# Optimization experiments

Measured on AMD Instinct MI355X. Metric: run time of the kernel, lower is better.

Reference implementation:

```python
import jax, jax.numpy as jnp
import numpy as np

B, T, IN, H, OUT = 1024, 512, 19, 128, 7


def setup_inputs() -> dict:
    key = jax.random.key(0)
    ks = jax.random.split(key, 12)
    k = 1.0 / np.sqrt(H)  # torch default init bound for LSTMCell/Linear
    u = lambda kk, shape: jax.random.uniform(kk, shape, jnp.float32, -k, k)
    return {
        "x": jax.random.normal(ks[0], (B, T, IN), jnp.float32),
        "W_ih1": u(ks[1], (4 * H, IN)),
        "W_hh1": u(ks[2], (4 * H, H)),
        "b_ih1": u(ks[3], (4 * H,)),
        "b_hh1": u(ks[4], (4 * H,)),
        "W_ih2": u(ks[5], (4 * H, H)),
        "W_hh2": u(ks[6], (4 * H, H)),
        "b_ih2": u(ks[7], (4 * H,)),
        "b_hh2": u(ks[8], (4 * H,)),
        "W_lin": u(ks[9], (OUT, H)),
        "b_lin": u(ks[10], (OUT,)),
    }


def _lstm_cell(x_t, h, c, W_ih, W_hh, b_ih, b_hh):
    # gates in torch order: i, f, g, o
    gates = x_t @ W_ih.T + b_ih + h @ W_hh.T + b_hh  # [B, 4H]
    i, f, g, o = jnp.split(gates, 4, axis=-1)
    c_new = jax.nn.sigmoid(f) * c + jax.nn.sigmoid(i) * jnp.tanh(g)
    h_new = jax.nn.sigmoid(o) * jnp.tanh(c_new)
    return h_new, c_new


def reference(x, W_ih1, W_hh1, b_ih1, b_hh1, W_ih2, W_hh2, b_ih2, b_hh2, W_lin, b_lin):
    n = x.shape[0]
    z = jnp.zeros((n, H), jnp.float32)

    def step(carry, x_t):
        h1, c1, h2, c2 = carry
        h1, c1 = _lstm_cell(x_t, h1, c1, W_ih1, W_hh1, b_ih1, b_hh1)
        h2, c2 = _lstm_cell(h1, h2, c2, W_ih2, W_hh2, b_ih2, b_hh2)
        y = h2 @ W_lin.T + b_lin  # [B, OUT]
        return (h1, c1, h2, c2), y

    xs = jnp.swapaxes(x, 0, 1)  # [T, B, IN]
    _, ys = jax.lax.scan(step, (z, z, z, z), xs)  # ys: [T, B, OUT]
    # torch.cat(outputs, 1) -> [B, T*OUT]
    return jnp.swapaxes(ys, 0, 1).reshape(n, -1)
```

## Files before the change

### kernel.cpp

```cpp
#include <hip/hip_runtime.h>


typedef _Float16 half8 __attribute__((ext_vector_type(8)));
typedef float f32x4 __attribute__((ext_vector_type(4)));

#define MFMA16(a, b, c) __builtin_amdgcn_mfma_f32_16x16x32_f16((a), (b), (c), 0, 0, 0)
#define BARRIER() asm volatile("s_waitcnt lgkmcnt(0)\ns_barrier" ::: "memory")

__device__ __forceinline__ void pin(half8& v) { asm volatile("" : "+v"(v)); }

__device__ __forceinline__ float sigf(float x) {
  return __builtin_amdgcn_rcpf(1.f + __expf(-x));
}
__device__ __forceinline__ float tanhf_(float x) {
  return 1.f - 2.f * __builtin_amdgcn_rcpf(1.f + __expf(2.f * x));
}
__device__ __forceinline__ float sel4(const f32x4 a, const int lg) {
  const float v01 = (lg & 1) ? a[1] : a[0];
  const float v23 = (lg & 1) ? a[3] : a[2];
  return (lg & 2) ? v23 : v01;
}

__global__ __launch_bounds__(512) void lstm_layer1_kernel(
    const float* __restrict__ x,
    const float* __restrict__ Wih,
    const float* __restrict__ Whh,
    const float* __restrict__ bih, const float* __restrict__ bhh,
    _Float16* __restrict__ h1g)
{
  __shared__ _Float16 xls[512][12][8];
  __shared__ _Float16 hbuf[2][64][8];
  const int tid = threadIdx.x, bid = blockIdx.x;
  const int wv = tid >> 6, lane = tid & 63;
  const int lg = lane >> 4, lc = lane & 15;
  const int col = wv * 16 + lc;
  const int off0 = lg * 32 + (lc & 3) * 8;
  const int woff = ((wv * 2 + (lc >> 3)) * 4 + lg) * 8 + (lc & 7);

  half8 wih_f[4], whh_f[4][4];
  float bias[4];
#pragma unroll
  for (int g = 0; g < 4; ++g) {
    const int n = g * 128 + col;
    bias[g] = bih[n] + bhh[n];
    half8 f;
#pragma unroll
    for (int j = 0; j < 8; ++j) {
      const int k = lg * 8 + j;
      f[j] = (_Float16)((k < 19) ? Wih[n * 19 + k] : 0.f);
    }
    wih_f[g] = f;
#pragma unroll
    for (int kk = 0; kk < 4; ++kk) {
      const float* p = Whh + n * 128 + kk * 32 + lg * 8;
      half8 f2;
#pragma unroll
      for (int j = 0; j < 8; ++j) f2[j] = (_Float16)p[j];
      whh_f[g][kk] = f2;
    }
  }

  for (int i2 = tid; i2 < 512 * 96; i2 += 512) {
    const int t = i2 / 96, r = i2 - t * 96;
    const int cc = r >> 5, rr = (r >> 3) & 3, j = r & 7;
    const int k = cc * 8 + j;
    float v = 0.f;
    if (k < 19) v = x[((size_t)(bid * 4 + rr) * 512 + t) * 19 + k];
    xls[t][cc * 4 + rr][j] = (_Float16)v;
  }
  for (int i = tid; i < 1024; i += 512) ((_Float16*)hbuf)[i] = (_Float16)0.f;
  __syncthreads();

  float c = 0.f;
  _Float16* h1p = h1g + (size_t)(bid * 4 + lg) * 128 + col;
  const _Float16* xb = &xls[0][0][0] + off0;
  _Float16* hb0p = &hbuf[0][0][0];
  const f32x4 fz = {0.f, 0.f, 0.f, 0.f};
  const bool xv = (lg < 3);

#define L1_STEP(T, RD, WR)                                                    \
  {                                                                           \
    const _Float16* rd = (RD) + off0;                                         \
    const half8 hb0 = *(const half8*)(rd);                                    \
    const half8 hb1 = *(const half8*)(rd + 128);                              \
    const half8 hb2 = *(const half8*)(rd + 256);                              \
    const half8 hb3 = *(const half8*)(rd + 384);                              \
    half8 ax = {};                                                            \
    if (xv) ax = *(const half8*)(xb + (T) * 96);                              \
    f32x4 a0 = MFMA16(ax, wih_f[0], fz);                                      \
    f32x4 a1 = MFMA16(ax, wih_f[1], fz);                                      \
    f32x4 a2 = MFMA16(ax, wih_f[2], fz);                                      \
    f32x4 a3 = MFMA16(ax, wih_f[3], fz);                                      \
    a0 = MFMA16(hb0, whh_f[0][0], a0); a1 = MFMA16(hb0, whh_f[1][0], a1);     \
    a2 = MFMA16(hb0, whh_f[2][0], a2); a3 = MFMA16(hb0, whh_f[3][0], a3);     \
    a0 = MFMA16(hb1, whh_f[0][1], a0); a1 = MFMA16(hb1, whh_f[1][1], a1);     \
    a2 = MFMA16(hb1, whh_f[2][1], a2); a3 = MFMA16(hb1, whh_f[3][1], a3);     \
    a0 = MFMA16(hb2, whh_f[0][2], a0); a1 = MFMA16(hb2, whh_f[1][2], a1);     \
    a2 = MFMA16(hb2, whh_f[2][2], a2); a3 = MFMA16(hb2, whh_f[3][2], a3);     \
    a0 = MFMA16(hb3, whh_f[0][3], a0); a1 = MFMA16(hb3, whh_f[1][3], a1);     \
    a2 = MFMA16(hb3, whh_f[2][3], a2); a3 = MFMA16(hb3, whh_f[3][3], a3);     \
    const float gi = sel4(a0, lg) + bias[0];                                  \
    const float gf = sel4(a1, lg) + bias[1];                                  \
    const float gg = sel4(a2, lg) + bias[2];                                  \
    const float go = sel4(a3, lg) + bias[3];                                  \
    const float I = sigf(gi), F = sigf(gf), G = tanhf_(gg), O = sigf(go);     \
    c = F * c + I * G;                                                        \
    const float h = O * tanhf_(c);                                            \
    const _Float16 h16 = (_Float16)h;                                         \
    (WR)[woff] = h16;                                                         \
    h1p[(size_t)(T) * 131072] = h16;                                          \
    BARRIER();                                                                \
  }

#pragma unroll 1
  for (int t = 0; t < 512; t += 2) {
    L1_STEP(t, hb0p + 512, hb0p);
    L1_STEP(t + 1, hb0p, hb0p + 512);
  }
#undef L1_STEP
}

__global__ __attribute__((amdgpu_waves_per_eu(2, 2))) __launch_bounds__(512)
void lstm_layer2_kernel(
    const _Float16* __restrict__ h1g,
    const float* __restrict__ Wih,
    const float* __restrict__ Whh,
    const float* __restrict__ bih, const float* __restrict__ bhh,
    const float* __restrict__ Wlin,
    const float* __restrict__ blin,
    float* __restrict__ out)
{
  __shared__ _Float16 hbuf[2][512];
  __shared__ _Float16 wlls[16][136];
  const int tid = threadIdx.x, bid = blockIdx.x;
  const int wv = tid >> 6, lane = tid & 63;
  const int lg = lane >> 4, lc = lane & 15;
  const int col = wv * 16 + lc;
  const int off0 = lg * 32 + (lc & 3) * 8;
  const int woff = ((col >> 3) * 4 + lg) * 8 + (col & 7);

  half8 wi_f[4][4], wh_f[4][4];
  float bias_s[4];
#pragma unroll
  for (int g = 0; g < 4; ++g) {
    const int n = g * 128 + col;
    bias_s[g] = bih[n] + bhh[n];
#pragma unroll
    for (int kk = 0; kk < 4; ++kk) {
      const float* pi = Wih + n * 128 + kk * 32 + lg * 8;
      const float* ph = Whh + n * 128 + kk * 32 + lg * 8;
      half8 fi, fh;
#pragma unroll
      for (int j = 0; j < 8; ++j) { fi[j] = (_Float16)pi[j]; fh[j] = (_Float16)ph[j]; }
      wi_f[g][kk] = fi;
      wh_f[g][kk] = fh;
    }
    pin(wi_f[g][0]); pin(wi_f[g][1]); pin(wi_f[g][2]); pin(wi_f[g][3]);
    pin(wh_f[g][0]); pin(wh_f[g][1]); pin(wh_f[g][2]); pin(wh_f[g][3]);
  }
  const f32x4 bV0 = {bias_s[0], bias_s[0], bias_s[0], bias_s[0]};
  const f32x4 bV1 = {bias_s[1], bias_s[1], bias_s[1], bias_s[1]};
  const f32x4 bV2 = {bias_s[2], bias_s[2], bias_s[2], bias_s[2]};
  const f32x4 bV3 = {bias_s[3], bias_s[3], bias_s[3], bias_s[3]};
  const bool yv = (lc < 7);
  const float ybias = yv ? blin[lc] : 0.f;
  const f32x4 ybV = {ybias, ybias, ybias, ybias};

  for (int i = tid; i < 16 * 128; i += 512)
    wlls[i >> 7][i & 127] = (_Float16)((i < 7 * 128) ? Wlin[i] : 0.f);
  for (int i = tid; i < 1024; i += 512) ((_Float16*)hbuf)[i] = (_Float16)0.f;
  __syncthreads();

  float c = 0.f;
  const _Float16* h1p = h1g + (size_t)(bid * 4 + (lc & 3)) * 128 + lg * 8;
  const f32x4 fz = {0.f, 0.f, 0.f, 0.f};
  half8 iC0 = *(const half8*)(h1p), iC1 = *(const half8*)(h1p + 32);
  half8 iC2 = *(const half8*)(h1p + 64), iC3 = *(const half8*)(h1p + 96);

#pragma unroll 1
  for (int t = 0; t < 512; ++t) {
    const int pb = t & 1;
    const _Float16* rd = &hbuf[pb ^ 1][0] + off0;
    const half8 hb0 = *(const half8*)(rd);
    const half8 hb1 = *(const half8*)(rd + 128);
    const half8 hb2 = *(const half8*)(rd + 256);
    const half8 hb3 = *(const half8*)(rd + 384);
    const size_t tn = (size_t)((t + 1 < 512) ? t + 1 : t) * 131072;
    const half8 iN0 = *(const half8*)(h1p + tn);
    const half8 iN1 = *(const half8*)(h1p + tn + 32);
    const half8 iN2 = *(const half8*)(h1p + tn + 64);
    const half8 iN3 = *(const half8*)(h1p + tn + 96);
    f32x4 a0 = MFMA16(iC0, wi_f[0][0], bV0);
    f32x4 a1 = MFMA16(iC0, wi_f[1][0], bV1);
    f32x4 a2 = MFMA16(iC0, wi_f[2][0], bV2);
    f32x4 a3 = MFMA16(iC0, wi_f[3][0], bV3);
    f32x4 b0 = MFMA16(hb0, wh_f[0][0], fz);
    f32x4 b1 = MFMA16(hb0, wh_f[1][0], fz);
    f32x4 b2 = MFMA16(hb0, wh_f[2][0], fz);
    f32x4 b3 = MFMA16(hb0, wh_f[3][0], fz);
    a0 = MFMA16(iC1, wi_f[0][1], a0); a1 = MFMA16(iC1, wi_f[1][1], a1);
    a2 = MFMA16(iC1, wi_f[2][1], a2); a3 = MFMA16(iC1, wi_f[3][1], a3);
    b0 = MFMA16(hb1, wh_f[0][1], b0); b1 = MFMA16(hb1, wh_f[1][1], b1);
    b2 = MFMA16(hb1, wh_f[2][1], b2); b3 = MFMA16(hb1, wh_f[3][1], b3);
    a0 = MFMA16(iC2, wi_f[0][2], a0); a1 = MFMA16(iC2, wi_f[1][2], a1);
    a2 = MFMA16(iC2, wi_f[2][2], a2); a3 = MFMA16(iC2, wi_f[3][2], a3);
    b0 = MFMA16(hb2, wh_f[0][2], b0); b1 = MFMA16(hb2, wh_f[1][2], b1);
    b2 = MFMA16(hb2, wh_f[2][2], b2); b3 = MFMA16(hb2, wh_f[3][2], b3);
    a0 = MFMA16(iC3, wi_f[0][3], a0); a1 = MFMA16(iC3, wi_f[1][3], a1);
    a2 = MFMA16(iC3, wi_f[2][3], a2); a3 = MFMA16(iC3, wi_f[3][3], a3);
    b0 = MFMA16(hb3, wh_f[0][3], b0); b1 = MFMA16(hb3, wh_f[1][3], b1);
    b2 = MFMA16(hb3, wh_f[2][3], b2); b3 = MFMA16(hb3, wh_f[3][3], b3);
    if (wv == 0 && t > 0) {
      const _Float16* wlp = &wlls[lc][0] + lg * 8;
      const half8 w0 = *(const half8*)(wlp);
      const half8 w1 = *(const half8*)(wlp + 32);
      const half8 w2 = *(const half8*)(wlp + 64);
      const half8 w3 = *(const half8*)(wlp + 96);
      f32x4 ya = ybV;
      ya = MFMA16(hb0, w0, ya);
      ya = MFMA16(hb1, w1, ya);
      ya = MFMA16(hb2, w2, ya);
      ya = MFMA16(hb3, w3, ya);
      if (lg == 0 && yv) {
#pragma unroll
        for (int j = 0; j < 4; ++j)
          out[(size_t)(bid * 4 + j) * 3584 + (size_t)(t - 1) * 7 + lc] = ya[j];
      }
    }
    const f32x4 s0 = a0 + b0, s1 = a1 + b1, s2 = a2 + b2, s3 = a3 + b3;
    const float gi = sel4(s0, lg), gf = sel4(s1, lg);
    const float gg = sel4(s2, lg), go = sel4(s3, lg);
    const float I = sigf(gi), F = sigf(gf), G = tanhf_(gg), O = sigf(go);
    c = F * c + I * G;
    hbuf[pb][woff] = (_Float16)(O * tanhf_(c));
    iC0 = iN0; iC1 = iN1; iC2 = iN2; iC3 = iN3;
    BARRIER();
  }

  if (wv == 0) {
    const _Float16* rd = &hbuf[1][0] + off0;
    const half8 hb0 = *(const half8*)(rd);
    const half8 hb1 = *(const half8*)(rd + 128);
    const half8 hb2 = *(const half8*)(rd + 256);
    const half8 hb3 = *(const half8*)(rd + 384);
    const _Float16* wlp = &wlls[lc][0] + lg * 8;
    const half8 w0 = *(const half8*)(wlp);
    const half8 w1 = *(const half8*)(wlp + 32);
    const half8 w2 = *(const half8*)(wlp + 64);
    const half8 w3 = *(const half8*)(wlp + 96);
    f32x4 ya = ybV;
    ya = MFMA16(hb0, w0, ya);
    ya = MFMA16(hb1, w1, ya);
    ya = MFMA16(hb2, w2, ya);
    ya = MFMA16(hb3, w3, ya);
    if (lg == 0 && yv) {
#pragma unroll
      for (int j = 0; j < 4; ++j)
        out[(size_t)(bid * 4 + j) * 3584 + (size_t)511 * 7 + lc] = ya[j];
    }
  }
}

extern "C" void kernel_launch(void* const* d_in, const int* in_sizes, int n_in,
                              void* d_out, int out_size, void* d_ws, size_t ws_size,
                              hipStream_t stream) {
  (void)in_sizes; (void)n_in; (void)out_size; (void)ws_size;
  const float* x     = (const float*)d_in[0];
  const float* W_ih1 = (const float*)d_in[1];
  const float* W_hh1 = (const float*)d_in[2];
  const float* b_ih1 = (const float*)d_in[3];
  const float* b_hh1 = (const float*)d_in[4];
  const float* W_ih2 = (const float*)d_in[5];
  const float* W_hh2 = (const float*)d_in[6];
  const float* b_ih2 = (const float*)d_in[7];
  const float* b_hh2 = (const float*)d_in[8];
  const float* W_lin = (const float*)d_in[9];
  const float* b_lin = (const float*)d_in[10];
  float* out = (float*)d_out;
  _Float16* h1g = (_Float16*)d_ws;

  lstm_layer1_kernel<<<256, 512, 0, stream>>>(x, W_ih1, W_hh1, b_ih1, b_hh1, h1g);
  lstm_layer2_kernel<<<256, 512, 0, stream>>>(h1g, W_ih2, W_hh2, b_ih2, b_hh2,
                                              W_lin, b_lin, out);
}
```

Baseline: 815.9 us.

## Split layer-2 LSTM into producer and consumer waves with an LDS ring

Layer 2 now runs 1024 threads per block. Eight producer waves compute the input projection W_ih·h1 a few steps ahead and write it as fp16 into a 5-slot shared-memory ring. Eight consumer waves then do only the recurrent W_hh MFMAs plus the gate math. This takes the input-projection MFMAs and global loads off the serial recurrence path, but it adds a block-wide barrier that spans twice as many waves. Rounding the pre-activations to fp16 also costs some precision.

```diff
diff --git a/kernel.cpp b/kernel.cpp
--- a/kernel.cpp
+++ b/kernel.cpp
@@ -2,10 +2,13 @@
 
 
 typedef _Float16 half8 __attribute__((ext_vector_type(8)));
+typedef _Float16 half4 __attribute__((ext_vector_type(4)));
 typedef float f32x4 __attribute__((ext_vector_type(4)));
 
 #define MFMA16(a, b, c) __builtin_amdgcn_mfma_f32_16x16x32_f16((a), (b), (c), 0, 0, 0)
 #define BARRIER() asm volatile("s_waitcnt lgkmcnt(0)\ns_barrier" ::: "memory")
+#define D_AHEAD 4
+#define NSLOT 5
 
 __device__ __forceinline__ void pin(half8& v) { asm volatile("" : "+v"(v)); }
 
@@ -120,8 +123,7 @@
 #undef L1_STEP
 }
 
-__global__ __attribute__((amdgpu_waves_per_eu(2, 2))) __launch_bounds__(512)
-void lstm_layer2_kernel(
+__global__ __launch_bounds__(1024) void lstm_layer2_pc(
     const _Float16* __restrict__ h1g,
     const float* __restrict__ Wih,
     const float* __restrict__ Whh,
@@ -130,133 +132,170 @@
     const float* __restrict__ blin,
     float* __restrict__ out)
 {
-  __shared__ _Float16 hbuf[2][512];
+  __shared__ _Float16 ring[NSLOT][2048];
+  __shared__ _Float16 h2b[2][512];
   __shared__ _Float16 wlls[16][136];
   const int tid = threadIdx.x, bid = blockIdx.x;
   const int wv = tid >> 6, lane = tid & 63;
   const int lg = lane >> 4, lc = lane & 15;
-  const int col = wv * 16 + lc;
+  const bool isCons = (wv < 8);
+  const int cw = isCons ? wv : (wv - 8);
+  const int col = cw * 16 + lc;
   const int off0 = lg * 32 + (lc & 3) * 8;
   const int woff = ((col >> 3) * 4 + lg) * 8 + (col & 7);
 
-  half8 wi_f[4][4], wh_f[4][4];
-  float bias_s[4];
-#pragma unroll
-  for (int g = 0; g < 4; ++g) {
-    const int n = g * 128 + col;
-    bias_s[g] = bih[n] + bhh[n];
-#pragma unroll
-    for (int kk = 0; kk < 4; ++kk) {
-      const float* pi = Wih + n * 128 + kk * 32 + lg * 8;
-      const float* ph = Whh + n * 128 + kk * 32 + lg * 8;
-      half8 fi, fh;
-#pragma unroll
-      for (int j = 0; j < 8; ++j) { fi[j] = (_Float16)pi[j]; fh[j] = (_Float16)ph[j]; }
-      wi_f[g][kk] = fi;
-      wh_f[g][kk] = fh;
-    }
-    pin(wi_f[g][0]); pin(wi_f[g][1]); pin(wi_f[g][2]); pin(wi_f[g][3]);
-    pin(wh_f[g][0]); pin(wh_f[g][1]); pin(wh_f[g][2]); pin(wh_f[g][3]);
-  }
-  const f32x4 bV0 = {bias_s[0], bias_s[0], bias_s[0], bias_s[0]};
-  const f32x4 bV1 = {bias_s[1], bias_s[1], bias_s[1], bias_s[1]};
-  const f32x4 bV2 = {bias_s[2], bias_s[2], bias_s[2], bias_s[2]};
-  const f32x4 bV3 = {bias_s[3], bias_s[3], bias_s[3], bias_s[3]};
-  const bool yv = (lc < 7);
-  const float ybias = yv ? blin[lc] : 0.f;
-  const f32x4 ybV = {ybias, ybias, ybias, ybias};
-
-  for (int i = tid; i < 16 * 128; i += 512)
+  for (int i = tid; i < 16 * 128; i += 1024)
     wlls[i >> 7][i & 127] = (_Float16)((i < 7 * 128) ? Wlin[i] : 0.f);
-  for (int i = tid; i < 1024; i += 512) ((_Float16*)hbuf)[i] = (_Float16)0.f;
-  __syncthreads();
-
-  float c = 0.f;
-  const _Float16* h1p = h1g + (size_t)(bid * 4 + (lc & 3)) * 128 + lg * 8;
-  const f32x4 fz = {0.f, 0.f, 0.f, 0.f};
-  half8 iC0 = *(const half8*)(h1p), iC1 = *(const half8*)(h1p + 32);
-  half8 iC2 = *(const half8*)(h1p + 64), iC3 = *(const half8*)(h1p + 96);
-
+  for (int i = tid; i < 1024; i += 1024) ((_Float16*)h2b)[i] = (_Float16)0.f;
+
+  if (isCons) {
+    half8 wh_f[4][4];
+#pragma unroll
+    for (int g = 0; g < 4; ++g) {
+      const int n = g * 128 + col;
+#pragma unroll
+      for (int kk = 0; kk < 4; ++kk) {
+        const float* p = Whh + n * 128 + kk * 32 + lg * 8;
+        half8 f;
+#pragma unroll
+        for (int j = 0; j < 8; ++j) f[j] = (_Float16)p[j];
+        wh_f[g][kk] = f;
+      }
+      pin(wh_f[g][0]); pin(wh_f[g][1]); pin(wh_f[g][2]); pin(wh_f[g][3]);
+    }
+    const bool yv = (lc < 7);
+    const float ybias = yv ? blin[lc] : 0.f;
+    __syncthreads();
+
+    float c = 0.f;
+    int slotR = 0;
 #pragma unroll 1
-  for (int t = 0; t < 512; ++t) {
-    const int pb = t & 1;
-    const _Float16* rd = &hbuf[pb ^ 1][0] + off0;
-    const half8 hb0 = *(const half8*)(rd);
-    const half8 hb1 = *(const half8*)(rd + 128);
-    const half8 hb2 = *(const half8*)(rd + 256);
-    const half8 hb3 = *(const half8*)(rd + 384);
-    const size_t tn = (size_t)((t + 1 < 512) ? t + 1 : t) * 131072;
-    const half8 iN0 = *(const half8*)(h1p + tn);
-    const half8 iN1 = *(const half8*)(h1p + tn + 32);
-    const half8 iN2 = *(const half8*)(h1p + tn + 64);
-    const half8 iN3 = *(const half8*)(h1p + tn + 96);
-    f32x4 a0 = MFMA16(iC0, wi_f[0][0], bV0);
-    f32x4 a1 = MFMA16(iC0, wi_f[1][0], bV1);
-    f32x4 a2 = MFMA16(iC0, wi_f[2][0], bV2);
-    f32x4 a3 = MFMA16(iC0, wi_f[3][0], bV3);
-    f32x4 b0 = MFMA16(hb0, wh_f[0][0], fz);
-    f32x4 b1 = MFMA16(hb0, wh_f[1][0], fz);
-    f32x4 b2 = MFMA16(hb0, wh_f[2][0], fz);
-    f32x4 b3 = MFMA16(hb0, wh_f[3][0], fz);
-    a0 = MFMA16(iC1, wi_f[0][1], a0); a1 = MFMA16(iC1, wi_f[1][1], a1);
-    a2 = MFMA16(iC1, wi_f[2][1], a2); a3 = MFMA16(iC1, wi_f[3][1], a3);
-    b0 = MFMA16(hb1, wh_f[0][1], b0); b1 = MFMA16(hb1, wh_f[1][1], b1);
-    b2 = MFMA16(hb1, wh_f[2][1], b2); b3 = MFMA16(hb1, wh_f[3][1], b3);
-    a0 = MFMA16(iC2, wi_f[0][2], a0); a1 = MFMA16(iC2, wi_f[1][2], a1);
-    a2 = MFMA16(iC2, wi_f[2][2], a2); a3 = MFMA16(iC2, wi_f[3][2], a3);
-    b0 = MFMA16(hb2, wh_f[0][2], b0); b1 = MFMA16(hb2, wh_f[1][2], b1);
-    b2 = MFMA16(hb2, wh_f[2][2], b2); b3 = MFMA16(hb2, wh_f[3][2], b3);
-    a0 = MFMA16(iC3, wi_f[0][3], a0); a1 = MFMA16(iC3, wi_f[1][3], a1);
-    a2 = MFMA16(iC3, wi_f[2][3], a2); a3 = MFMA16(iC3, wi_f[3][3], a3);
-    b0 = MFMA16(hb3, wh_f[0][3], b0); b1 = MFMA16(hb3, wh_f[1][3], b1);
-    b2 = MFMA16(hb3, wh_f[2][3], b2); b3 = MFMA16(hb3, wh_f[3][3], b3);
-    if (wv == 0 && t > 0) {
+    for (int it = 0; it < 512 + D_AHEAD; ++it) {
+      if (it >= D_AHEAD) {
+        const int t = it - D_AHEAD;
+        const int pb = t & 1;
+        const _Float16* rd = &h2b[pb ^ 1][0] + off0;
+        const half8 q0 = *(const half8*)(rd);
+        const half8 q1 = *(const half8*)(rd + 128);
+        const half8 q2 = *(const half8*)(rd + 256);
+        const half8 q3 = *(const half8*)(rd + 384);
+        const _Float16* rp = &ring[slotR][0] + (col << 2);
+        const half4 r0 = *(const half4*)(rp);
+        const half4 r1 = *(const half4*)(rp + 512);
+        const half4 r2 = *(const half4*)(rp + 1024);
+        const half4 r3 = *(const half4*)(rp + 1536);
+        f32x4 a0 = {(float)r0[0], (float)r0[1], (float)r0[2], (float)r0[3]};
+        f32x4 a1 = {(float)r1[0], (float)r1[1], (float)r1[2], (float)r1[3]};
+        f32x4 a2 = {(float)r2[0], (float)r2[1], (float)r2[2], (float)r2[3]};
+        f32x4 a3 = {(float)r3[0], (float)r3[1], (float)r3[2], (float)r3[3]};
+        a0 = MFMA16(q0, wh_f[0][0], a0); a1 = MFMA16(q0, wh_f[1][0], a1);
+        a2 = MFMA16(q0, wh_f[2][0], a2); a3 = MFMA16(q0, wh_f[3][0], a3);
+        a0 = MFMA16(q1, wh_f[0][1], a0); a1 = MFMA16(q1, wh_f[1][1], a1);
+        a2 = MFMA16(q1, wh_f[2][1], a2); a3 = MFMA16(q1, wh_f[3][1], a3);
+        a0 = MFMA16(q2, wh_f[0][2], a0); a1 = MFMA16(q2, wh_f[1][2], a1);
+        a2 = MFMA16(q2, wh_f[2][2], a2); a3 = MFMA16(q2, wh_f[3][2], a3);
+        a0 = MFMA16(q3, wh_f[0][3], a0); a1 = MFMA16(q3, wh_f[1][3], a1);
+        a2 = MFMA16(q3, wh_f[2][3], a2); a3 = MFMA16(q3, wh_f[3][3], a3);
+        if (wv == 0 && t > 0) {
+          const _Float16* wlp = &wlls[lc][0] + lg * 8;
+          f32x4 ya = {ybias, ybias, ybias, ybias};
+          {
+            const half8 w0 = *(const half8*)(wlp);
+            const half8 w1 = *(const half8*)(wlp + 32);
+            ya = MFMA16(q0, w0, ya);
+            ya = MFMA16(q1, w1, ya);
+          }
+          {
+            const half8 w2 = *(const half8*)(wlp + 64);
+            const half8 w3 = *(const half8*)(wlp + 96);
+            ya = MFMA16(q2, w2, ya);
+            ya = MFMA16(q3, w3, ya);
+          }
+          if (lg == 0 && yv) {
+#pragma unroll
+            for (int j = 0; j < 4; ++j)
+              out[(size_t)(bid * 4 + j) * 3584 + (size_t)(t - 1) * 7 + lc] = ya[j];
+          }
+        }
+        const float gi = sel4(a0, lg), gf = sel4(a1, lg);
+        const float gg = sel4(a2, lg), go = sel4(a3, lg);
+        const float I = sigf(gi), F = sigf(gf), G = tanhf_(gg), O = sigf(go);
+        c = F * c + I * G;
+        h2b[pb][woff] = (_Float16)(O * tanhf_(c));
+        if (++slotR == NSLOT) slotR = 0;
+      }
+      BARRIER();
+    }
+    if (wv == 0) {
+      const _Float16* rd = &h2b[1][0] + off0;
+      const half8 q0 = *(const half8*)(rd);
+      const half8 q1 = *(const half8*)(rd + 128);
+      const half8 q2 = *(const half8*)(rd + 256);
+      const half8 q3 = *(const half8*)(rd + 384);
       const _Float16* wlp = &wlls[lc][0] + lg * 8;
       const half8 w0 = *(const half8*)(wlp);
       const half8 w1 = *(const half8*)(wlp + 32);
       const half8 w2 = *(const half8*)(wlp + 64);
       const half8 w3 = *(const half8*)(wlp + 96);
-      f32x4 ya = ybV;
-      ya = MFMA16(hb0, w0, ya);
-      ya = MFMA16(hb1, w1, ya);
-      ya = MFMA16(hb2, w2, ya);
-      ya = MFMA16(hb3, w3, ya);
+      f32x4 ya = {ybias, ybias, ybias, ybias};
+      ya = MFMA16(q0, w0, ya);
+      ya = MFMA16(q1, w1, ya);
+      ya = MFMA16(q2, w2, ya);
+      ya = MFMA16(q3, w3, ya);
       if (lg == 0 && yv) {
 #pragma unroll
         for (int j = 0; j < 4; ++j)
-          out[(size_t)(bid * 4 + j) * 3584 + (size_t)(t - 1) * 7 + lc] = ya[j];
-      }
-    }
-    const f32x4 s0 = a0 + b0, s1 = a1 + b1, s2 = a2 + b2, s3 = a3 + b3;
-    const float gi = sel4(s0, lg), gf = sel4(s1, lg);
-    const float gg = sel4(s2, lg), go = sel4(s3, lg);
-    const float I = sigf(gi), F = sigf(gf), G = tanhf_(gg), O = sigf(go);
-    c = F * c + I * G;
-    hbuf[pb][woff] = (_Float16)(O * tanhf_(c));
-    iC0 = iN0; iC1 = iN1; iC2 = iN2; iC3 = iN3;
-    BARRIER();
-  }
-
-  if (wv == 0) {
-    const _Float16* rd = &hbuf[1][0] + off0;
-    const half8 hb0 = *(const half8*)(rd);
-    const half8 hb1 = *(const half8*)(rd + 128);
-    const half8 hb2 = *(const half8*)(rd + 256);
-    const half8 hb3 = *(const half8*)(rd + 384);
-    const _Float16* wlp = &wlls[lc][0] + lg * 8;
-    const half8 w0 = *(const half8*)(wlp);
-    const half8 w1 = *(const half8*)(wlp + 32);
-    const half8 w2 = *(const half8*)(wlp + 64);
-    const half8 w3 = *(const half8*)(wlp + 96);
-    f32x4 ya = ybV;
-    ya = MFMA16(hb0, w0, ya);
-    ya = MFMA16(hb1, w1, ya);
-    ya = MFMA16(hb2, w2, ya);
-    ya = MFMA16(hb3, w3, ya);
-    if (lg == 0 && yv) {
-#pragma unroll
-      for (int j = 0; j < 4; ++j)
-        out[(size_t)(bid * 4 + j) * 3584 + (size_t)511 * 7 + lc] = ya[j];
+          out[(size_t)(bid * 4 + j) * 3584 + (size_t)511 * 7 + lc] = ya[j];
+      }
+    }
+  } else {
+    half8 wi_f[4][4];
+    float bias_s[4];
+#pragma unroll
+    for (int g = 0; g < 4; ++g) {
+      const int n = g * 128 + col;
+      bias_s[g] = bih[n] + bhh[n];
+#pragma unroll
+      for (int kk = 0; kk < 4; ++kk) {
+        const float* p = Wih + n * 128 + kk * 32 + lg * 8;
+        half8 f;
+#pragma unroll
+        for (int j = 0; j < 8; ++j) f[j] = (_Float16)p[j];
+        wi_f[g][kk] = f;
+      }
+      pin(wi_f[g][0]); pin(wi_f[g][1]); pin(wi_f[g][2]); pin(wi_f[g][3]);
+    }
+    __syncthreads();
+
+    const _Float16* h1p = h1g + (size_t)(bid * 4 + (lc & 3)) * 128 + lg * 8;
+    const bool wr = (lg == 0);
+    int slotW = 0;
+#pragma unroll 1
+    for (int it = 0; it < 512 + D_AHEAD; ++it) {
+      if (it < 512) {
+        const _Float16* hp = h1p + (size_t)it * 131072;
+        const half8 p0 = *(const half8*)(hp);
+        const half8 p1 = *(const half8*)(hp + 32);
+        const half8 p2 = *(const half8*)(hp + 64);
+        const half8 p3 = *(const half8*)(hp + 96);
+        _Float16* wp_ = &ring[slotW][0] + (col << 2);
+#pragma unroll
+        for (int g = 0; g < 4; ++g) {
+          f32x4 a = {bias_s[g], bias_s[g], bias_s[g], bias_s[g]};
+          a = MFMA16(p0, wi_f[g][0], a);
+          a = MFMA16(p1, wi_f[g][1], a);
+          a = MFMA16(p2, wi_f[g][2], a);
+          a = MFMA16(p3, wi_f[g][3], a);
+          if (wr) {
+            half4 h4;
+#pragma unroll
+            for (int j = 0; j < 4; ++j) h4[j] = (_Float16)a[j];
+            *(half4*)(wp_ + g * 512) = h4;
+          }
+        }
+        if (++slotW == NSLOT) slotW = 0;
+      }
+      BARRIER();
     }
   }
 }
@@ -280,6 +319,6 @@
   _Float16* h1g = (_Float16*)d_ws;
 
   lstm_layer1_kernel<<<256, 512, 0, stream>>>(x, W_ih1, W_hh1, b_ih1, b_hh1, h1g);
-  lstm_layer2_kernel<<<256, 512, 0, stream>>>(h1g, W_ih2, W_hh2, b_ih2, b_hh2,
-                                              W_lin, b_lin, out);
-}
+  lstm_layer2_pc<<<256, 1024, 0, stream>>>(h1g, W_ih2, W_hh2, b_ih2, b_hh2,
+                                           W_lin, b_lin, out);
+}
```

Measured after the change: 1.018 ms. 1.25x slower.
